# Performance work log

Measured on AMD Instinct MI355X. Metric: run time of the kernel, lower is better.

The kernel has to match this reference:

```python
import jax, jax.numpy as jnp
import numpy as np

HIDDEN_DIM = 64
VOCAB_SIZE = 64
MEMORY_SLOTS = 8
SEQ_LEN = 32
B = 32768


def setup_inputs() -> dict:
    key = jax.random.key(0)
    ks = jax.random.split(key, 11)
    s = 0.1
    return {
        "seqs": jax.random.randint(ks[0], (B, SEQ_LEN), 0, VOCAB_SIZE),
        "query_tok": jax.random.randint(ks[1], (B,), 0, VOCAB_SIZE),
        "embed_table": jax.random.normal(ks[2], (VOCAB_SIZE + 2, HIDDEN_DIM), jnp.float32) * s,
        "sc_w1": jax.random.normal(ks[3], (HIDDEN_DIM, 32), jnp.float32) * s,
        "sc_b1": jax.random.normal(ks[4], (32,), jnp.float32) * s,
        "sc_w2": jax.random.normal(ks[5], (32, 1), jnp.float32) * s,
        "sc_b2": jax.random.normal(ks[6], (1,), jnp.float32) * s,
        "rh_w1": jax.random.normal(ks[7], (2 * HIDDEN_DIM, HIDDEN_DIM), jnp.float32) * s,
        "rh_b1": jax.random.normal(ks[8], (HIDDEN_DIM,), jnp.float32) * s,
        "rh_w2": jax.random.normal(ks[9], (HIDDEN_DIM, VOCAB_SIZE), jnp.float32) * s,
        "rh_b2": jax.random.normal(ks[10], (VOCAB_SIZE,), jnp.float32) * s,
    }


def reference(seqs, query_tok, embed_table, sc_w1, sc_b1, sc_w2, sc_b2,
              rh_w1, rh_b1, rh_w2, rh_b2):
    # Embed the first SEQ_LEN-1 tokens: [B, 31, H]
    embs = embed_table[seqs[:, : SEQ_LEN - 1]]
    slot_ids = jnp.arange(MEMORY_SLOTS)

    def scan_one(embs_b):
        def step(carry, emb):
            mem, count = carry  # mem: [8, H], count: scalar int32
            # score all slots (harmless during fill phase; only used when full)
            scores = (jnp.maximum(mem @ sc_w1 + sc_b1, 0.0) @ sc_w2 + sc_b2)[:, 0]
            evict_idx = jnp.argmin(scores)
            # full: pop evict_idx (shift left above it), append new emb at slot 7
            rolled = jnp.roll(mem, -1, axis=0)
            full_mem = jnp.where(slot_ids[:, None] < evict_idx, mem, rolled)
            full_mem = full_mem.at[MEMORY_SLOTS - 1].set(emb)
            # filling: write new emb at position `count`
            fill_mem = mem.at[jnp.clip(count, 0, MEMORY_SLOTS - 1)].set(emb)
            new_mem = jnp.where(count >= MEMORY_SLOTS, full_mem, fill_mem)
            new_count = jnp.minimum(count + 1, MEMORY_SLOTS)
            return (new_mem, new_count), None

        init = (jnp.zeros((MEMORY_SLOTS, HIDDEN_DIM), embs_b.dtype),
                jnp.array(0, jnp.int32))
        (mem, _), _ = jax.lax.scan(step, init, embs_b)
        return mem.mean(0)  # memory is always full (31 tokens > 8 slots)

    mem_summary = jax.vmap(scan_one)(embs)  # [B, H]
    q_emb = embed_table[query_tok]          # [B, H]
    h = jnp.concatenate([q_emb, mem_summary], axis=-1)  # [B, 2H]
    return jnp.maximum(h @ rh_w1 + rh_b1, 0.0) @ rh_w2 + rh_b2  # [B, VOCAB]
```

## Files before the change

### kernel.cpp

```cpp
#include <hip/hip_runtime.h>


#define SEQ_LEN 32
#define MEM_SLOTS 8

#define WS_SCORE 0
#define WS_Q1B   64
#define WS_M1S   (64 + 4096)

__global__ __launch_bounds__(256) void lem_precompute(
    const float* __restrict__ embed,
    const float* __restrict__ sc_w1, const float* __restrict__ sc_b1,
    const float* __restrict__ sc_w2, const float* __restrict__ sc_b2,
    const float* __restrict__ rh_w1, const float* __restrict__ rh_b1,
    float* __restrict__ ws)
{
    const int t = threadIdx.x;
    if (blockIdx.x < 16) {
        const int p = blockIdx.x * 256 + t;
        const int v = p >> 6, k = p & 63;
        const float* e = embed + v * 64;
        float q = rh_b1[k];
        float m = 0.f;
        #pragma unroll 8
        for (int i = 0; i < 64; ++i) {
            q = fmaf(e[i], rh_w1[i * 64 + k], q);
            m = fmaf(e[i], rh_w1[(64 + i) * 64 + k], m);
        }
        ws[WS_Q1B + p] = q;
        ws[WS_M1S + p] = m * 0.125f;
    } else {
        __shared__ float part[2048];
        #pragma unroll
        for (int r = 0; r < 8; ++r) {
            const int s = r * 256 + t;
            const int v = s >> 5, k = s & 31;
            const float* e = embed + v * 64;
            float a = sc_b1[k];
            #pragma unroll 8
            for (int i = 0; i < 64; ++i) a = fmaf(e[i], sc_w1[i * 32 + k], a);
            a = fmaxf(a, 0.f);
            part[s] = a * sc_w2[k];
        }
        __syncthreads();
        if (t < 64) {
            float s = sc_b2[0];
            for (int k = 0; k < 32; ++k) s += part[t * 32 + k];
            ws[WS_SCORE + t] = s;
        }
    }
}

__global__ __launch_bounds__(256) void lem_main(
    const int* __restrict__ seqs, const int* __restrict__ qtok,
    const float* __restrict__ rh_w2, const float* __restrict__ rh_b2,
    const float* __restrict__ ws, float* __restrict__ out)
{
    __shared__ float QM[4096];
    __shared__ float MM[4096];
    __shared__ float score_s[64];
    __shared__ unsigned long long tok_s[64];
    __shared__ float hh[64 * 65];

    const int t = threadIdx.x;
    const int gbase = blockIdx.x * 64;

    for (int i = t; i < 4096; i += 256) {
        QM[i] = ws[WS_Q1B + i];
        MM[i] = ws[WS_M1S + i];
    }
    if (t < 64) score_s[t] = ws[WS_SCORE + t];
    __syncthreads();

    if (t < 64) {
        const int b = gbase + t;
        int tk[SEQ_LEN];
        const int4* sq4 = (const int4*)(seqs + (long long)b * SEQ_LEN);
        #pragma unroll
        for (int r = 0; r < SEQ_LEN / 4; ++r) {
            int4 v = sq4[r];
            tk[r * 4 + 0] = v.x; tk[r * 4 + 1] = v.y;
            tk[r * 4 + 2] = v.z; tk[r * 4 + 3] = v.w;
        }
        int tok[MEM_SLOTS]; float sc[MEM_SLOTS];
        #pragma unroll
        for (int j = 0; j < MEM_SLOTS; ++j) tok[j] = tk[j];
        #pragma unroll
        for (int j = 0; j < MEM_SLOTS; ++j) sc[j] = score_s[tok[j]];
        #pragma unroll
        for (int step = MEM_SLOTS; step < SEQ_LEN - 1; ++step) {
            const int nt = tk[step];
            const float ns = score_s[nt];
            float bv = sc[0]; int be = 0;
            #pragma unroll
            for (int j = 1; j < MEM_SLOTS; ++j) {
                const bool lt = sc[j] < bv;
                bv = lt ? sc[j] : bv;
                be = lt ? j : be;
            }
            #pragma unroll
            for (int j = 0; j < MEM_SLOTS - 1; ++j) {
                const bool take = (j >= be);
                sc[j]  = take ? sc[j + 1]  : sc[j];
                tok[j] = take ? tok[j + 1] : tok[j];
            }
            sc[MEM_SLOTS - 1] = ns;
            tok[MEM_SLOTS - 1] = nt;
        }
        unsigned long long pk = 0ull;
        #pragma unroll
        for (int j = 0; j < MEM_SLOTS; ++j)
            pk |= (unsigned long long)(tok[j] & 255) << (8 * j);
        tok_s[t] = pk;
    }
    __syncthreads();

    const int lane = t & 63;
    const int w = t >> 6;
    const int k0 = w * 16;
    const int b = lane;
    const int qb = qtok[gbase + b];
    const unsigned long long pk = tok_s[b];

    float acc[16];
    const float4* QM4 = (const float4*)QM;
    const float4* MM4 = (const float4*)MM;
    {
        const int qbase = (qb * 64 + k0) >> 2;
        #pragma unroll
        for (int j4 = 0; j4 < 4; ++j4) {
            float4 v = QM4[qbase + j4];
            acc[j4 * 4 + 0] = v.x; acc[j4 * 4 + 1] = v.y;
            acc[j4 * 4 + 2] = v.z; acc[j4 * 4 + 3] = v.w;
        }
    }
    #pragma unroll
    for (int j = 0; j < MEM_SLOTS; ++j) {
        const int tkn = (int)((pk >> (8 * j)) & 255);
        const int mb = (tkn * 64 + k0) >> 2;
        #pragma unroll
        for (int j4 = 0; j4 < 4; ++j4) {
            float4 v = MM4[mb + j4];
            acc[j4 * 4 + 0] += v.x; acc[j4 * 4 + 1] += v.y;
            acc[j4 * 4 + 2] += v.z; acc[j4 * 4 + 3] += v.w;
        }
    }
    #pragma unroll
    for (int j = 0; j < 16; ++j)
        hh[b * 65 + k0 + j] = fmaxf(acc[j], 0.f);
    __syncthreads();

    const int m0 = __builtin_amdgcn_readfirstlane(k0);
    float o[16];
    #pragma unroll
    for (int j = 0; j < 16; ++j) o[j] = rh_b2[m0 + j];
    #pragma unroll 4
    for (int k = 0; k < 64; ++k) {
        const float h = hh[b * 65 + k];
        #pragma unroll
        for (int j = 0; j < 16; ++j)
            o[j] = fmaf(h, rh_w2[k * 64 + m0 + j], o[j]);
    }
    float4* op4 = (float4*)(out + (long long)(gbase + b) * 64 + m0);
    #pragma unroll
    for (int j4 = 0; j4 < 4; ++j4)
        op4[j4] = make_float4(o[j4 * 4 + 0], o[j4 * 4 + 1],
                              o[j4 * 4 + 2], o[j4 * 4 + 3]);
}

extern "C" void kernel_launch(void* const* d_in, const int* in_sizes, int n_in,
                              void* d_out, int out_size, void* d_ws, size_t ws_size,
                              hipStream_t stream)
{
    const int*   seqs   = (const int*)d_in[0];
    const int*   qtok   = (const int*)d_in[1];
    const float* embed  = (const float*)d_in[2];
    const float* sc_w1  = (const float*)d_in[3];
    const float* sc_b1  = (const float*)d_in[4];
    const float* sc_w2  = (const float*)d_in[5];
    const float* sc_b2  = (const float*)d_in[6];
    const float* rh_w1  = (const float*)d_in[7];
    const float* rh_b1  = (const float*)d_in[8];
    const float* rh_w2  = (const float*)d_in[9];
    const float* rh_b2  = (const float*)d_in[10];
    float* out = (float*)d_out;
    float* ws  = (float*)d_ws;

    const int B = in_sizes[1];

    lem_precompute<<<17, 256, 0, stream>>>(embed, sc_w1, sc_b1, sc_w2, sc_b2,
                                           rh_w1, rh_b1, ws);
    lem_main<<<B / 64, 256, 0, stream>>>(seqs, qtok, rh_w2, rh_b2, ws, out);
}
```

Measured before the change: 108.2 us.

## Transpose memory projection table in LDS and read query projection from global

The precompute kernel now stores the memory-side projection table transposed (k-major), and the main kernel stages only that table in shared memory. The query-side table is read directly from global/L2 instead of being copied to LDS. The gather over the memory tokens becomes scalar LDS reads indexed by token, and the hidden buffer is laid out k-major so per-lane accesses are consecutive. The aim is to cut LDS staging traffic and shared-memory footprint, which may allow more resident blocks, and to reduce bank conflicts. In exchange it issues 16 scalar LDS loads per slot instead of 4 vector loads, and the query lookup becomes a random global gather.

```diff
diff --git a/kernel.cpp b/kernel.cpp
--- a/kernel.cpp
+++ b/kernel.cpp
@@ -6,7 +6,7 @@
 
 #define WS_SCORE 0
 #define WS_Q1B   64
-#define WS_M1S   (64 + 4096)
+#define WS_M1T   (64 + 4096)
 
 __global__ __launch_bounds__(256) void lem_precompute(
     const float* __restrict__ embed,
@@ -27,8 +27,8 @@
             q = fmaf(e[i], rh_w1[i * 64 + k], q);
             m = fmaf(e[i], rh_w1[(64 + i) * 64 + k], m);
         }
-        ws[WS_Q1B + p] = q;
-        ws[WS_M1S + p] = m * 0.125f;
+        ws[WS_Q1B + v * 64 + k] = q;
+        ws[WS_M1T + k * 64 + v] = m * 0.125f;
     } else {
         __shared__ float part[2048];
         #pragma unroll
@@ -56,19 +56,15 @@
     const float* __restrict__ rh_w2, const float* __restrict__ rh_b2,
     const float* __restrict__ ws, float* __restrict__ out)
 {
-    __shared__ float QM[4096];
-    __shared__ float MM[4096];
+    __shared__ float MT[4096];
     __shared__ float score_s[64];
     __shared__ unsigned long long tok_s[64];
-    __shared__ float hh[64 * 65];
+    __shared__ float hh[4096];
 
     const int t = threadIdx.x;
     const int gbase = blockIdx.x * 64;
 
-    for (int i = t; i < 4096; i += 256) {
-        QM[i] = ws[WS_Q1B + i];
-        MM[i] = ws[WS_M1S + i];
-    }
+    for (int i = t; i < 4096; i += 256) MT[i] = ws[WS_M1T + i];
     if (t < 64) score_s[t] = ws[WS_SCORE + t];
     __syncthreads();
 
@@ -123,13 +119,12 @@
     const unsigned long long pk = tok_s[b];
 
     float acc[16];
-    const float4* QM4 = (const float4*)QM;
-    const float4* MM4 = (const float4*)MM;
     {
+        const float4* Q4 = (const float4*)(ws + WS_Q1B);
         const int qbase = (qb * 64 + k0) >> 2;
         #pragma unroll
         for (int j4 = 0; j4 < 4; ++j4) {
-            float4 v = QM4[qbase + j4];
+            float4 v = Q4[qbase + j4];
             acc[j4 * 4 + 0] = v.x; acc[j4 * 4 + 1] = v.y;
             acc[j4 * 4 + 2] = v.z; acc[j4 * 4 + 3] = v.w;
         }
@@ -137,17 +132,13 @@
     #pragma unroll
     for (int j = 0; j < MEM_SLOTS; ++j) {
         const int tkn = (int)((pk >> (8 * j)) & 255);
-        const int mb = (tkn * 64 + k0) >> 2;
         #pragma unroll
-        for (int j4 = 0; j4 < 4; ++j4) {
-            float4 v = MM4[mb + j4];
-            acc[j4 * 4 + 0] += v.x; acc[j4 * 4 + 1] += v.y;
-            acc[j4 * 4 + 2] += v.z; acc[j4 * 4 + 3] += v.w;
-        }
+        for (int jj = 0; jj < 16; ++jj)
+            acc[jj] += MT[(k0 + jj) * 64 + tkn];
     }
     #pragma unroll
-    for (int j = 0; j < 16; ++j)
-        hh[b * 65 + k0 + j] = fmaxf(acc[j], 0.f);
+    for (int jj = 0; jj < 16; ++jj)
+        hh[(k0 + jj) * 64 + b] = fmaxf(acc[jj], 0.f);
     __syncthreads();
 
     const int m0 = __builtin_amdgcn_readfirstlane(k0);
@@ -156,7 +147,7 @@
     for (int j = 0; j < 16; ++j) o[j] = rh_b2[m0 + j];
     #pragma unroll 4
     for (int k = 0; k < 64; ++k) {
-        const float h = hh[b * 65 + k];
+        const float h = hh[k * 64 + b];
         #pragma unroll
         for (int j = 0; j < 16; ++j)
             o[j] = fmaf(h, rh_w2[k * 64 + m0 + j], o[j]);
```

Result: faster. 101.5 us (-6.2%).
